# Kernel optimization log

Hardware: AMD Instinct MI355X
Metric: run time of the kernel (lower is better)

Reference implementation:

```python
import jax, jax.numpy as jnp
import numpy as np
from functools import partial

EPS = 1e-5
SCALE = 2
NUM_BLOCKS = 2


def _layernorm(x, g, b):
    mu = jnp.mean(x, axis=-1, keepdims=True)
    var = jnp.var(x, axis=-1, keepdims=True)
    return (x - mu) * jax.lax.rsqrt(var + EPS) * g + b


def _rwkv(tokens, td, Wk, Wv, Wr, Wo, ln_g, ln_b):
    # tokens: (B, N, C)
    x = _layernorm(tokens, ln_g, ln_b)
    k = jnp.einsum('bnc,oc->bno', x, Wk)
    v = jnp.einsum('bnc,oc->bno', x, Wv)
    r = jax.nn.sigmoid(jnp.einsum('bnc,oc->bno', x, Wr))
    decay = jnp.exp(-jax.nn.relu(td))  # (C,)

    def step(state, inp):
        kt, vt, rt = inp  # each (B, C)
        state = state * decay + kt
        return state, rt * (state + vt)

    B, N, C = tokens.shape
    init = jnp.zeros((B, C), dtype=tokens.dtype)
    # scan over token axis
    _, yT = jax.lax.scan(step, init, (k.transpose(1, 0, 2), v.transpose(1, 0, 2), r.transpose(1, 0, 2)))
    y = yT.transpose(1, 0, 2)  # (B, N, C)
    return jnp.einsum('bnc,oc->bno', y, Wo)


def reference(x, global_state, cond_gw, cond_gb, cond_bw, cond_bb,
              td, Wk, Wv, Wr, Wo, ln_g, ln_b, gp_w, gp_b, bp_w, bp_b):
    B, C, H, W = x.shape
    Hp, Wp = H * SCALE, W * SCALE
    # bilinear upsample, half-pixel centers == torch align_corners=False
    x_up = jax.image.resize(x, (B, C, Hp, Wp), method='bilinear')
    tokens = x_up.reshape(B, C, Hp * Wp).transpose(0, 2, 1)  # (B, N, C)
    # semantic conditioning (FiLM from global state)
    gamma = (global_state @ cond_gw.T + cond_gb)[:, None, :]
    beta = (global_state @ cond_bw.T + cond_bb)[:, None, :]
    tokens = tokens * (1.0 + gamma) + beta

    out = x_up
    cur = tokens
    for i in range(NUM_BLOCKS):
        if i > 0:
            cur = out.reshape(B, C, Hp * Wp).transpose(0, 2, 1)
        t = _rwkv(cur, td[i], Wk[i], Wv[i], Wr[i], Wo[i], ln_g[i], ln_b[i])
        g = jnp.einsum('bnc,oc->bno', t, gp_w[i]) + gp_b[i]
        bt = jnp.einsum('bnc,oc->bno', t, bp_w[i]) + bp_b[i]
        g = g.transpose(0, 2, 1).reshape(B, C, Hp, Wp)
        bt = bt.transpose(0, 2, 1).reshape(B, C, Hp, Wp)
        out = out * (1.0 + jnp.tanh(g)) + bt
    return out


def setup_inputs() -> dict:
    key = jax.random.key(0)
    ks = jax.random.split(key, 16)
    B, C, H, W = 8, 128, 64, 64
    w_scale = 0.02
    inp = {
        'x': jax.random.normal(ks[0], (B, C, H, W), jnp.float32),
        'global_state': jax.random.normal(ks[1], (B, C), jnp.float32),
        'cond_gw': jax.random.normal(ks[2], (C, C), jnp.float32) * w_scale,
        'cond_gb': jnp.zeros((C,), jnp.float32),
        'cond_bw': jax.random.normal(ks[3], (C, C), jnp.float32) * w_scale,
        'cond_bb': jnp.zeros((C,), jnp.float32),
        'td': jax.random.uniform(ks[4], (NUM_BLOCKS, C), jnp.float32),
        'Wk': jax.random.normal(ks[5], (NUM_BLOCKS, C, C), jnp.float32) * w_scale,
        'Wv': jax.random.normal(ks[6], (NUM_BLOCKS, C, C), jnp.float32) * w_scale,
        'Wr': jax.random.normal(ks[7], (NUM_BLOCKS, C, C), jnp.float32) * w_scale,
        'Wo': jax.random.normal(ks[8], (NUM_BLOCKS, C, C), jnp.float32) * w_scale,
        'ln_g': jnp.ones((NUM_BLOCKS, C), jnp.float32),
        'ln_b': jnp.zeros((NUM_BLOCKS, C), jnp.float32),
        'gp_w': jax.random.normal(ks[9], (NUM_BLOCKS, C, C), jnp.float32) * w_scale,
        'gp_b': jnp.zeros((NUM_BLOCKS, C), jnp.float32),
        'bp_w': jax.random.normal(ks[10], (NUM_BLOCKS, C, C), jnp.float32) * w_scale,
        'bp_b': jnp.zeros((NUM_BLOCKS, C), jnp.float32),
    }
    return inp
```

## Files before the change

kernel.cpp:

```cpp
#include <hip/hip_runtime.h>
#include <hip/hip_bf16.h>

#define BB 8
#define CC 128
#define NN 16384
#define MM (BB * NN)
#define NCH 128
#define CLN 128

typedef __attribute__((ext_vector_type(8))) short short8;
typedef __attribute__((ext_vector_type(4))) float floatx4;
typedef unsigned short u16;
typedef unsigned int u32;

__device__ __forceinline__ float bf2f(u16 h) {
  u32 u = ((u32)h) << 16;
  return __builtin_bit_cast(float, u);
}
__device__ __forceinline__ u16 f2bf(float f) {
  u32 u = __builtin_bit_cast(u32, f);
  u32 r = u + 0x7FFFu + ((u >> 16) & 1u);
  return (u16)(r >> 16);
}

__global__ void film_kernel(const float* __restrict__ gs, const float* __restrict__ gw,
                            const float* __restrict__ gb, const float* __restrict__ bw,
                            const float* __restrict__ bb, float* __restrict__ gamma,
                            float* __restrict__ beta) {
  int idx = blockIdx.x * 256 + threadIdx.x;
  int b = idx >> 7, c = idx & 127;
  float sg = 0.f, sb = 0.f;
  for (int j = 0; j < 128; ++j) {
    float g = gs[b * 128 + j];
    sg += g * gw[c * 128 + j];
    sb += g * bw[c * 128 + j];
  }
  gamma[idx] = sg + gb[c];
  beta[idx] = sb + bb[c];
}

__global__ void convert_kernel(const float* __restrict__ Wk, const float* __restrict__ Wv,
                               const float* __restrict__ Wr, const float* __restrict__ Wo,
                               const float* __restrict__ gp, const float* __restrict__ bp,
                               u16* __restrict__ dst) {
  int idx = blockIdx.x * 256 + threadIdx.x;
  int which = idx >> 15;
  int off = idx & 32767;
  const float* s;
  switch (which) {
    case 0: s = Wk; break; case 1: s = Wv; break; case 2: s = Wr; break;
    case 3: s = Wo; break; case 4: s = gp; break; default: s = bp; break;
  }
  dst[idx] = f2bf(s[off]);
}

template <int UPS>
__global__ __launch_bounds__(256) void prep_kernel(
    const float* __restrict__ src, const float* __restrict__ gamma,
    const float* __restrict__ beta, const float* __restrict__ lng,
    const float* __restrict__ lnb, float* __restrict__ outp, u16* __restrict__ xn) {
  __shared__ float tile[64][129];
  __shared__ float smu[64], srs[64];
  int bidx = blockIdx.x;
  int half = bidx & 1;
  int ho = (bidx >> 1) & 127;
  int b = bidx >> 8;
  int wo0 = half * 64;
  int tid = threadIdx.x;
  int tk = tid & 63;
  int wo = wo0 + tk;
  int c0 = tid >> 6;
  int j0 = 0, j1 = 0, i0 = 0, i1 = 0;
  float wy0 = 0.f, wy1 = 0.f, wx0 = 0.f, wx1 = 0.f;
  if (UPS) {
    int jj = ho >> 1;
    if ((ho & 1) == 0) { j0 = jj > 0 ? jj - 1 : 0; j1 = jj; wy0 = 0.25f; wy1 = 0.75f; }
    else               { j0 = jj; j1 = jj < 63 ? jj + 1 : 63; wy0 = 0.75f; wy1 = 0.25f; }
    int ii = wo >> 1;
    if ((wo & 1) == 0) { i0 = ii > 0 ? ii - 1 : 0; i1 = ii; wx0 = 0.25f; wx1 = 0.75f; }
    else               { i0 = ii; i1 = ii < 63 ? ii + 1 : 63; wx0 = 0.75f; wx1 = 0.25f; }
  }
  for (int it = 0; it < 32; ++it) {
    int c = it * 4 + c0;
    float v;
    if (UPS) {
      const float* xp = src + ((size_t)(b * 128 + c)) * 4096;
      v = wy0 * (wx0 * xp[j0 * 64 + i0] + wx1 * xp[j0 * 64 + i1]) +
          wy1 * (wx0 * xp[j1 * 64 + i0] + wx1 * xp[j1 * 64 + i1]);
      outp[((size_t)(b * 128 + c)) * 16384 + ho * 128 + wo] = v;
      v = v * (1.f + gamma[b * 128 + c]) + beta[b * 128 + c];
    } else {
      v = src[((size_t)(b * 128 + c)) * 16384 + ho * 128 + wo];
    }
    tile[tk][c] = v;
  }
  __syncthreads();
  {
    int token = tid >> 2, q = tid & 3;
    float s = 0.f, s2 = 0.f;
    for (int j = 0; j < 32; ++j) { float v = tile[token][q * 32 + j]; s += v; s2 += v * v; }
    s += __shfl_xor(s, 1); s2 += __shfl_xor(s2, 1);
    s += __shfl_xor(s, 2); s2 += __shfl_xor(s2, 2);
    if (q == 0) {
      float mu = s * 0.0078125f;
      float var = s2 * 0.0078125f - mu * mu;
      smu[token] = mu;
      srs[token] = rsqrtf(var + 1e-5f);
    }
  }
  __syncthreads();
  size_t base = ((size_t)b * 16384 + ho * 128 + wo0) * 128;
  for (int it = 0; it < 32; ++it) {
    int idx = it * 256 + tid;
    int token = idx >> 7, c = idx & 127;
    float v = (tile[token][c] - smu[token]) * srs[token] * lng[c] + lnb[c];
    xn[base + idx] = f2bf(v);
  }
}

__global__ __launch_bounds__(256) void gemm_S_kernel(
    const u16* __restrict__ A, const u16* __restrict__ W0,
    const float* __restrict__ td, float* __restrict__ Sbuf) {
  __shared__ u16 Alds[128 * 128];
  __shared__ float Sred[512];
  int tid = threadIdx.x;
  int wave = tid >> 6, lane = tid & 63;
  int l15 = lane & 15, l4 = lane >> 4;
  size_t row0 = (size_t)blockIdx.x * 128;
#pragma unroll
  for (int it = 0; it < 8; ++it) {
    int idx = it * 256 + tid;
    int rr = idx >> 4, s = idx & 15;
    uint4 d = *(const uint4*)(A + (row0 + rr) * 128 + s * 8);
    *(uint4*)(&Alds[rr * 128 + ((s ^ (rr & 15)) << 3)]) = d;
  }
  __syncthreads();
  floatx4 acc[2][8];
#pragma unroll
  for (int mi = 0; mi < 2; ++mi)
#pragma unroll
    for (int ni = 0; ni < 8; ++ni) acc[mi][ni] = (floatx4){0.f, 0.f, 0.f, 0.f};
#pragma unroll
  for (int kk = 0; kk < 4; ++kk) {
    int seg = kk * 4 + l4;
    short8 a0 = *(const short8*)(&Alds[(wave * 32 + l15) * 128 + ((seg ^ l15) << 3)]);
    short8 a1 = *(const short8*)(&Alds[(wave * 32 + 16 + l15) * 128 + ((seg ^ l15) << 3)]);
#pragma unroll
    for (int ni = 0; ni < 8; ++ni) {
      short8 bfr = *(const short8*)(W0 + (ni * 16 + l15) * 128 + kk * 32 + l4 * 8);
      acc[0][ni] = __builtin_amdgcn_mfma_f32_16x16x32_bf16(a0, bfr, acc[0][ni], 0, 0, 0);
      acc[1][ni] = __builtin_amdgcn_mfma_f32_16x16x32_bf16(a1, bfr, acc[1][ni], 0, 0, 0);
    }
  }
  int T0 = wave * 32 + l4 * 4;
#pragma unroll
  for (int ni = 0; ni < 8; ++ni) {
    int c = ni * 16 + l15;
    float a = fmaxf(td[c], 0.f);
    float E = __expf(-a * (float)(127 - T0));
    float r1 = __expf(a);
    float r16 = __expf(a * 16.f);
    float w = E, sum;
    sum  = w * acc[0][ni][0]; w *= r1;
    sum += w * acc[0][ni][1]; w *= r1;
    sum += w * acc[0][ni][2]; w *= r1;
    sum += w * acc[0][ni][3];
    w = E * r16;
    sum += w * acc[1][ni][0]; w *= r1;
    sum += w * acc[1][ni][1]; w *= r1;
    sum += w * acc[1][ni][2]; w *= r1;
    sum += w * acc[1][ni][3];
    sum += __shfl_xor(sum, 16);
    sum += __shfl_xor(sum, 32);
    if (l4 == 0) Sred[wave * 128 + c] = sum;
  }
  __syncthreads();
  if (tid < 128) {
    float s = Sred[tid] + Sred[128 + tid] + Sred[256 + tid] + Sred[384 + tid];
    Sbuf[(blockIdx.x & 127) * 1024 + (blockIdx.x >> 7) * 128 + tid] = s;
  }
}

__global__ __launch_bounds__(256) void scan2_kernel(const float* __restrict__ S,
                                                    const float* __restrict__ td,
                                                    float* __restrict__ init) {
  int wave = threadIdx.x >> 6, lane = threadIdx.x & 63;
  int bc = blockIdx.x * 4 + wave;
  int c = bc & 127;
  float a1 = __expf(-fmaxf(td[c], 0.f) * 128.f);
  float s0 = S[(2 * lane) * 1024 + bc];
  float s1 = S[(2 * lane + 1) * 1024 + bc];
  float s = s1 + a1 * s0;
  float a = a1 * a1;
  for (int off = 1; off < 64; off <<= 1) {
    float ss = __shfl_up(s, off);
    float aa = __shfl_up(a, off);
    if (lane >= off) { s = s + a * ss; a = a * aa; }
  }
  float e = __shfl_up(s, 1);
  if (lane == 0) e = 0.f;
  init[(2 * lane) * 1024 + bc] = e;
  init[(2 * lane + 1) * 1024 + bc] = a1 * e + s0;
}

__global__ __launch_bounds__(256) void gemm_y_kernel(
    const u16* __restrict__ A, const u16* __restrict__ Wv_, const u16* __restrict__ Wr_,
    const u16* __restrict__ Wk_, const float* __restrict__ td,
    const float* __restrict__ init_, u16* __restrict__ outY) {
  __shared__ u16 Alds[128 * 128];
  __shared__ u16 Wlds[128 * 128];
  __shared__ float SWT[512];
  __shared__ float ILS[128];
  int tid = threadIdx.x;
  int wave = tid >> 6, lane = tid & 63;
  int l15 = lane & 15, l4 = lane >> 4;
  size_t row0 = (size_t)blockIdx.x * 128;
  int bI = blockIdx.x >> 7, chunkI = blockIdx.x & 127;
  if (tid < 128) ILS[tid] = init_[chunkI * 1024 + bI * 128 + tid];

#pragma unroll
  for (int it = 0; it < 8; ++it) {
    int idx = it * 256 + tid;
    int rr = idx >> 4, s = idx & 15;
    uint4 d = *(const uint4*)(A + (row0 + rr) * 128 + s * 8);
    *(uint4*)(&Alds[rr * 128 + ((s ^ (rr & 15)) << 3)]) = d;
  }
#pragma unroll
  for (int it = 0; it < 8; ++it) {
    int idx = it * 256 + tid;
    int rr = idx >> 4, s = idx & 15;
    uint4 d = *(const uint4*)(Wv_ + rr * 128 + s * 8);
    *(uint4*)(&Wlds[rr * 128 + ((s ^ (rr & 15)) << 3)]) = d;
  }
  float dd[8], d4a[8];
#pragma unroll
  for (int ni = 0; ni < 8; ++ni) {
    float a = fmaxf(td[ni * 16 + l15], 0.f);
    float d = __expf(-a);
    dd[ni] = d;
    float d2 = d * d;
    d4a[ni] = d2 * d2;
  }
  __syncthreads();

  floatx4 accv[2][8];
#pragma unroll
  for (int mi = 0; mi < 2; ++mi)
#pragma unroll
    for (int ni = 0; ni < 8; ++ni) accv[mi][ni] = (floatx4){0.f, 0.f, 0.f, 0.f};
#pragma unroll
  for (int kk = 0; kk < 4; ++kk) {
    int seg = kk * 4 + l4;
    short8 a0 = *(const short8*)(&Alds[(wave * 32 + l15) * 128 + ((seg ^ l15) << 3)]);
    short8 a1 = *(const short8*)(&Alds[(wave * 32 + 16 + l15) * 128 + ((seg ^ l15) << 3)]);
#pragma unroll
    for (int ni = 0; ni < 8; ++ni) {
      short8 bfr = *(const short8*)(&Wlds[(ni * 16 + l15) * 128 + ((seg ^ l15) << 3)]);
      accv[0][ni] = __builtin_amdgcn_mfma_f32_16x16x32_bf16(a0, bfr, accv[0][ni], 0, 0, 0);
      accv[1][ni] = __builtin_amdgcn_mfma_f32_16x16x32_bf16(a1, bfr, accv[1][ni], 0, 0, 0);
    }
  }
  __syncthreads();
#pragma unroll
  for (int it = 0; it < 8; ++it) {
    int idx = it * 256 + tid;
    int rr = idx >> 4, s = idx & 15;
    uint4 d = *(const uint4*)(Wr_ + rr * 128 + s * 8);
    *(uint4*)(&Wlds[rr * 128 + ((s ^ (rr & 15)) << 3)]) = d;
  }
  __syncthreads();
  floatx4 accr[2][8];
#pragma unroll
  for (int mi = 0; mi < 2; ++mi)
#pragma unroll
    for (int ni = 0; ni < 8; ++ni) accr[mi][ni] = (floatx4){0.f, 0.f, 0.f, 0.f};
#pragma unroll
  for (int kk = 0; kk < 4; ++kk) {
    int seg = kk * 4 + l4;
    short8 a0 = *(const short8*)(&Alds[(wave * 32 + l15) * 128 + ((seg ^ l15) << 3)]);
    short8 a1 = *(const short8*)(&Alds[(wave * 32 + 16 + l15) * 128 + ((seg ^ l15) << 3)]);
#pragma unroll
    for (int ni = 0; ni < 8; ++ni) {
      short8 bfr = *(const short8*)(&Wlds[(ni * 16 + l15) * 128 + ((seg ^ l15) << 3)]);
      accr[0][ni] = __builtin_amdgcn_mfma_f32_16x16x32_bf16(a0, bfr, accr[0][ni], 0, 0, 0);
      accr[1][ni] = __builtin_amdgcn_mfma_f32_16x16x32_bf16(a1, bfr, accr[1][ni], 0, 0, 0);
    }
  }
  u32 rvp[2][8][2], rp[2][8][2];
#pragma unroll
  for (int mi = 0; mi < 2; ++mi) {
#pragma unroll
    for (int ni = 0; ni < 8; ++ni) {
      float rs[4], rv[4];
#pragma unroll
      for (int j = 0; j < 4; ++j) {
        float sg = 1.f / (1.f + __expf(-accr[mi][ni][j]));
        rs[j] = sg;
        rv[j] = sg * accv[mi][ni][j];
      }
      rvp[mi][ni][0] = (u32)f2bf(rv[0]) | ((u32)f2bf(rv[1]) << 16);
      rvp[mi][ni][1] = (u32)f2bf(rv[2]) | ((u32)f2bf(rv[3]) << 16);
      rp[mi][ni][0] = (u32)f2bf(rs[0]) | ((u32)f2bf(rs[1]) << 16);
      rp[mi][ni][1] = (u32)f2bf(rs[2]) | ((u32)f2bf(rs[3]) << 16);
    }
  }
  __syncthreads();
#pragma unroll
  for (int it = 0; it < 8; ++it) {
    int idx = it * 256 + tid;
    int rr = idx >> 4, s = idx & 15;
    uint4 d = *(const uint4*)(Wk_ + rr * 128 + s * 8);
    *(uint4*)(&Wlds[rr * 128 + ((s ^ (rr & 15)) << 3)]) = d;
  }
  __syncthreads();
  floatx4 acck[2][8];
#pragma unroll
  for (int mi = 0; mi < 2; ++mi)
#pragma unroll
    for (int ni = 0; ni < 8; ++ni) acck[mi][ni] = (floatx4){0.f, 0.f, 0.f, 0.f};
#pragma unroll
  for (int kk = 0; kk < 4; ++kk) {
    int seg = kk * 4 + l4;
    short8 a0 = *(const short8*)(&Alds[(wave * 32 + l15) * 128 + ((seg ^ l15) << 3)]);
    short8 a1 = *(const short8*)(&Alds[(wave * 32 + 16 + l15) * 128 + ((seg ^ l15) << 3)]);
#pragma unroll
    for (int ni = 0; ni < 8; ++ni) {
      short8 bfr = *(const short8*)(&Wlds[(ni * 16 + l15) * 128 + ((seg ^ l15) << 3)]);
      acck[0][ni] = __builtin_amdgcn_mfma_f32_16x16x32_bf16(a0, bfr, acck[0][ni], 0, 0, 0);
      acck[1][ni] = __builtin_amdgcn_mfma_f32_16x16x32_bf16(a1, bfr, acck[1][ni], 0, 0, 0);
    }
  }
  float Elr[2][8];
  float B0r[8];
#pragma unroll
  for (int ni = 0; ni < 8; ++ni) {
    float d = dd[ni], d4 = d4a[ni];
    float d8 = d4 * d4, d16 = d8 * d8;
    float I[2];
#pragma unroll
    for (int mi = 0; mi < 2; ++mi) {
      float p0 = acck[mi][ni][0];
      float p1 = d * p0 + acck[mi][ni][1];
      float p2 = d * p1 + acck[mi][ni][2];
      float p3 = d * p2 + acck[mi][ni][3];
      acck[mi][ni][0] = p0; acck[mi][ni][1] = p1;
      acck[mi][ni][2] = p2; acck[mi][ni][3] = p3;
      float Iv = p3;
      float t1 = __shfl_up(Iv, 16);
      if (l4 >= 1) Iv += d4 * t1;
      float t2 = __shfl_up(Iv, 32);
      if (l4 >= 2) Iv += d8 * t2;
      float ex = __shfl_up(Iv, 16);
      Elr[mi][ni] = (l4 == 0) ? 0.f : ex;
      I[mi] = Iv;
    }
    float B0 = __shfl(I[0], 48 + l15);
    float B1 = __shfl(I[1], 48 + l15);
    B0r[ni] = B0;
    if (l4 == 0) SWT[wave * 128 + ni * 16 + l15] = B1 + d16 * B0;
  }
  __syncthreads();
  u16* YW = Wlds;
#pragma unroll
  for (int ni = 0; ni < 8; ++ni) {
    int c = ni * 16 + l15;
    float d = dd[ni], d4 = d4a[ni];
    float d8 = d4 * d4, d12 = d8 * d4, d16 = d8 * d8, d32 = d16 * d16;
    float e = ILS[c];
#pragma unroll
    for (int wv = 0; wv < 3; ++wv)
      if (wv < wave) e = e * d32 + SWT[wv * 128 + c];
    float d4l = (l4 == 0) ? 1.f : ((l4 == 1) ? d4 : ((l4 == 2) ? d8 : d12));
#pragma unroll
    for (int mi = 0; mi < 2; ++mi) {
      float Emi = (mi == 0) ? e : (e * d16 + B0r[ni]);
      float Sb = Elr[mi][ni] + d4l * Emi;
      float w = d;
#pragma unroll
      for (int j = 0; j < 4; ++j) {
        float s = acck[mi][ni][j] + w * Sb;
        w *= d;
        float rvv = bf2f((u16)(rvp[mi][ni][j >> 1] >> ((j & 1) * 16)));
        float rss = bf2f((u16)(rp[mi][ni][j >> 1] >> ((j & 1) * 16)));
        float y = rvv + rss * s;
        int row = wave * 32 + mi * 16 + l4 * 4 + j;
        int colsw = c ^ (((row >> 2) & 3) << 4);
        YW[row * 128 + colsw] = f2bf(y);
      }
    }
  }
  __syncthreads();
#pragma unroll
  for (int it = 0; it < 8; ++it) {
    int idx = it * 256 + tid;
    int row = idx >> 4, cb = (idx & 15) * 8;
    int csw = cb ^ (((row >> 2) & 3) << 4);
    uint4 dv = *(const uint4*)(&YW[row * 128 + csw]);
    *(uint4*)(outY + (row0 + row) * 128 + cb) = dv;
  }
}

__global__ __launch_bounds__(512, 4) void tail_kernel(
    const u16* __restrict__ yl,
    const u16* __restrict__ Wo, const u16* __restrict__ Wg, const u16* __restrict__ Wb,
    const float* __restrict__ gpb, const float* __restrict__ bpb,
    float* __restrict__ outp) {
  __shared__ u32 SMEM[8192];
  u16* Y = (u16*)SMEM;
  u16* T2 = (u16*)SMEM;
  u32* MB = SMEM;

  int tid = threadIdx.x;
  int wave = tid >> 6, lane = tid & 63;
  int l15 = lane & 15, l4 = lane >> 4;
  int b = blockIdx.x >> 7;
  int chunk = blockIdx.x & 127;
  size_t ebase = ((size_t)b * 16384 + (size_t)chunk * 128) * 128;

#pragma unroll
  for (int it = 0; it < 4; ++it) {
    int idx = it * 512 + tid;
    int t = idx >> 4;
    int c8 = (idx & 15) * 8;
    uint4 yv = *(const uint4*)(yl + ebase + (size_t)t * 128 + c8);
    *(uint4*)(&Y[t * 128 + (((c8 >> 3) ^ (t & 15)) << 3)]) = yv;
  }
  __syncthreads();

  int ob = wave * 16;
  short8 wof[4];
#pragma unroll
  for (int kk = 0; kk < 4; ++kk)
    wof[kk] = *(const short8*)(Wo + (ob + l15) * 128 + kk * 32 + l4 * 8);
  floatx4 acc[8];
#pragma unroll
  for (int ni = 0; ni < 8; ++ni) acc[ni] = (floatx4){0.f, 0.f, 0.f, 0.f};
#pragma unroll
  for (int kk = 0; kk < 4; ++kk) {
    int seg = kk * 4 + l4;
#pragma unroll
    for (int ni = 0; ni < 8; ++ni) {
      short8 yf = *(const short8*)(&Y[(ni * 16 + l15) * 128 + ((seg ^ l15) << 3)]);
      acc[ni] = __builtin_amdgcn_mfma_f32_16x16x32_bf16(wof[kk], yf, acc[ni], 0, 0, 0);
    }
  }
  __syncthreads();

#pragma unroll
  for (int ni = 0; ni < 8; ++ni) {
    int tok = ni * 16 + l15;
#pragma unroll
    for (int j = 0; j < 4; j += 2) {
      int o = ob + l4 * 4 + j;
      u32 pack = (u32)f2bf(acc[ni][j]) | ((u32)f2bf(acc[ni][j + 1]) << 16);
      int pos = tok * 128 + ((((o >> 3) ^ (tok & 15)) << 3) | (o & 7));
      *(u32*)(T2 + pos) = pack;
    }
  }
  __syncthreads();

  short8 wgf[4], wbf2[4];
#pragma unroll
  for (int kk = 0; kk < 4; ++kk) {
    wgf[kk]  = *(const short8*)(Wg + (ob + l15) * 128 + kk * 32 + l4 * 8);
    wbf2[kk] = *(const short8*)(Wb + (ob + l15) * 128 + kk * 32 + l4 * 8);
  }
  floatx4 ag[8], ab[8];
#pragma unroll
  for (int ni = 0; ni < 8; ++ni) {
    ag[ni] = (floatx4){0.f, 0.f, 0.f, 0.f};
    ab[ni] = (floatx4){0.f, 0.f, 0.f, 0.f};
  }
#pragma unroll
  for (int kk = 0; kk < 4; ++kk) {
    int seg = kk * 4 + l4;
#pragma unroll
    for (int ni = 0; ni < 8; ++ni) {
      short8 tf = *(const short8*)(&T2[(ni * 16 + l15) * 128 + ((seg ^ l15) << 3)]);
      ag[ni] = __builtin_amdgcn_mfma_f32_16x16x32_bf16(wgf[kk], tf, ag[ni], 0, 0, 0);
      ab[ni] = __builtin_amdgcn_mfma_f32_16x16x32_bf16(wbf2[kk], tf, ab[ni], 0, 0, 0);
    }
  }
  __syncthreads();

#pragma unroll
  for (int h = 0; h < 2; ++h) {
    if ((wave >> 2) == h) {
      int orel0 = (wave & 3) * 16;
#pragma unroll
      for (int ni = 0; ni < 8; ++ni) {
        int tok = ni * 16 + l15;
#pragma unroll
        for (int j = 0; j < 4; ++j) {
          int orel = orel0 + l4 * 4 + j;
          int o = h * 64 + orel;
          float g = ag[ni][j] + gpb[o];
          float t1 = __expf(2.f * g);
          float m = 2.f - 2.f / (t1 + 1.f);
          float bt = ab[ni][j] + bpb[o];
          int rot = ((orel & 3) << 2) | ((orel >> 2) & 3);
          MB[orel * 128 + ((((tok >> 3) ^ rot) << 3) | (tok & 7))] =
              (u32)f2bf(m) | ((u32)f2bf(bt) << 16);
        }
      }
    }
    __syncthreads();
#pragma unroll
    for (int it = 0; it < 2; ++it) {
      int idx = it * 512 + tid;
      int orel = idx >> 4, seg = idx & 15;
      int o = h * 64 + orel;
      int rot = ((orel & 3) << 2) | ((orel >> 2) & 3);
      int sp = ((seg ^ rot) << 3);
      uint4 mb0 = *(const uint4*)(&MB[orel * 128 + sp]);
      uint4 mb1 = *(const uint4*)(&MB[orel * 128 + sp + 4]);
      float* op = outp + ((size_t)(b * 128 + o)) * 16384 + chunk * 128 + seg * 8;
      float4 o0 = *(float4*)op;
      float4 o1 = *(float4*)(op + 4);
      o0.x = o0.x * bf2f((u16)(mb0.x & 0xffff)) + bf2f((u16)(mb0.x >> 16));
      o0.y = o0.y * bf2f((u16)(mb0.y & 0xffff)) + bf2f((u16)(mb0.y >> 16));
      o0.z = o0.z * bf2f((u16)(mb0.z & 0xffff)) + bf2f((u16)(mb0.z >> 16));
      o0.w = o0.w * bf2f((u16)(mb0.w & 0xffff)) + bf2f((u16)(mb0.w >> 16));
      o1.x = o1.x * bf2f((u16)(mb1.x & 0xffff)) + bf2f((u16)(mb1.x >> 16));
      o1.y = o1.y * bf2f((u16)(mb1.y & 0xffff)) + bf2f((u16)(mb1.y >> 16));
      o1.z = o1.z * bf2f((u16)(mb1.z & 0xffff)) + bf2f((u16)(mb1.z >> 16));
      o1.w = o1.w * bf2f((u16)(mb1.w & 0xffff)) + bf2f((u16)(mb1.w >> 16));
      *(float4*)op = o0;
      *(float4*)(op + 4) = o1;
    }
    __syncthreads();
  }
}

extern "C" void kernel_launch(void* const* d_in, const int* in_sizes, int n_in,
                              void* d_out, int out_size, void* d_ws, size_t ws_size,
                              hipStream_t stream) {
  const float* x        = (const float*)d_in[0];
  const float* gs       = (const float*)d_in[1];
  const float* cond_gw  = (const float*)d_in[2];
  const float* cond_gb  = (const float*)d_in[3];
  const float* cond_bw  = (const float*)d_in[4];
  const float* cond_bb  = (const float*)d_in[5];
  const float* td       = (const float*)d_in[6];
  const float* Wk       = (const float*)d_in[7];
  const float* Wv       = (const float*)d_in[8];
  const float* Wr       = (const float*)d_in[9];
  const float* Wo       = (const float*)d_in[10];
  const float* ln_g     = (const float*)d_in[11];
  const float* ln_b     = (const float*)d_in[12];
  const float* gp_w     = (const float*)d_in[13];
  const float* gp_b     = (const float*)d_in[14];
  const float* bp_w     = (const float*)d_in[15];
  const float* bp_b     = (const float*)d_in[16];
  float* outp = (float*)d_out;

  char* w = (char*)d_ws;
  float* gamma = (float*)w; w += 4096;
  float* beta  = (float*)w; w += 4096;
  u16* wbf     = (u16*)w;   w += 6 * 2 * 16384 * sizeof(u16);
  u16* xn      = (u16*)w;   w += (size_t)MM * 128 * sizeof(u16);
  u16* ybuf    = (u16*)w;   w += (size_t)MM * 128 * sizeof(u16);
  float* Sbuf  = (float*)w; w += NCH * 1024 * sizeof(float);
  float* ibuf  = (float*)w; w += NCH * 1024 * sizeof(float);

  film_kernel<<<4, 256, 0, stream>>>(gs, cond_gw, cond_gb, cond_bw, cond_bb, gamma, beta);
  convert_kernel<<<768, 256, 0, stream>>>(Wk, Wv, Wr, Wo, gp_w, bp_w, wbf);

  for (int blk = 0; blk < 2; ++blk) {
    const u16* bWk = wbf + 0 * 32768 + blk * 16384;
    const u16* bWv = wbf + 1 * 32768 + blk * 16384;
    const u16* bWr = wbf + 2 * 32768 + blk * 16384;
    const u16* bWo = wbf + 3 * 32768 + blk * 16384;
    const u16* bGp = wbf + 4 * 32768 + blk * 16384;
    const u16* bBp = wbf + 5 * 32768 + blk * 16384;
    const float* tdi = td + blk * 128;

    if (blk == 0)
      prep_kernel<1><<<2048, 256, 0, stream>>>(x, gamma, beta, ln_g, ln_b, outp, xn);
    else
      prep_kernel<0><<<2048, 256, 0, stream>>>(outp, nullptr, nullptr, ln_g + 128,
                                               ln_b + 128, nullptr, xn);

    gemm_S_kernel<<<1024, 256, 0, stream>>>(xn, bWk, tdi, Sbuf);
    scan2_kernel<<<256, 256, 0, stream>>>(Sbuf, tdi, ibuf);
    gemm_y_kernel<<<1024, 256, 0, stream>>>(xn, bWv, bWr, bWk, tdi, ibuf, ybuf);
    tail_kernel<<<1024, 512, 0, stream>>>(ybuf, bWo, bGp, bBp,
                                          gp_b + blk * 128, bp_b + blk * 128, outp);
  }
}
```

Measured before the change: 320.5 us.

## Halve scan chunk length and retile gemm_y to 64-row blocks with per-wave channels

The chunked linear-recurrence scan now uses 64-token chunks instead of 128. gemm_S emits two half-chunk sums per block and stages Wk in LDS. scan2 combines four chunk sums per lane, and gemm_y runs 2048 blocks of 64 rows, each wave owning 32 output channels. This removes the cross-wave SWT reduction, the LDS weight staging in gemm_y and its extra syncs, and lowers LDS use to raise occupancy. In exchange, each wave reads weights directly from global/L2, and intermediate s and r values are packed to bf16 before the final combine.

```diff
diff --git a/kernel.cpp b/kernel.cpp
--- a/kernel.cpp
+++ b/kernel.cpp
@@ -5,8 +5,8 @@
 #define CC 128
 #define NN 16384
 #define MM (BB * NN)
-#define NCH 128
-#define CLN 128
+#define NCH 256
+#define CLN 64
 
 typedef __attribute__((ext_vector_type(8))) short short8;
 typedef __attribute__((ext_vector_type(4))) float floatx4;
@@ -122,6 +122,7 @@
     const u16* __restrict__ A, const u16* __restrict__ W0,
     const float* __restrict__ td, float* __restrict__ Sbuf) {
   __shared__ u16 Alds[128 * 128];
+  __shared__ u16 Wlds[128 * 128];
   __shared__ float Sred[512];
   int tid = threadIdx.x;
   int wave = tid >> 6, lane = tid & 63;
@@ -134,6 +135,13 @@
     uint4 d = *(const uint4*)(A + (row0 + rr) * 128 + s * 8);
     *(uint4*)(&Alds[rr * 128 + ((s ^ (rr & 15)) << 3)]) = d;
   }
+#pragma unroll
+  for (int it = 0; it < 8; ++it) {
+    int idx = it * 256 + tid;
+    int rr = idx >> 4, s = idx & 15;
+    uint4 d = *(const uint4*)(W0 + rr * 128 + s * 8);
+    *(uint4*)(&Wlds[rr * 128 + ((s ^ (rr & 15)) << 3)]) = d;
+  }
   __syncthreads();
   floatx4 acc[2][8];
 #pragma unroll
@@ -147,17 +155,17 @@
     short8 a1 = *(const short8*)(&Alds[(wave * 32 + 16 + l15) * 128 + ((seg ^ l15) << 3)]);
 #pragma unroll
     for (int ni = 0; ni < 8; ++ni) {
-      short8 bfr = *(const short8*)(W0 + (ni * 16 + l15) * 128 + kk * 32 + l4 * 8);
+      short8 bfr = *(const short8*)(&Wlds[(ni * 16 + l15) * 128 + ((seg ^ l15) << 3)]);
       acc[0][ni] = __builtin_amdgcn_mfma_f32_16x16x32_bf16(a0, bfr, acc[0][ni], 0, 0, 0);
       acc[1][ni] = __builtin_amdgcn_mfma_f32_16x16x32_bf16(a1, bfr, acc[1][ni], 0, 0, 0);
     }
   }
-  int T0 = wave * 32 + l4 * 4;
+  int T0h = (wave & 1) * 32 + l4 * 4;
 #pragma unroll
   for (int ni = 0; ni < 8; ++ni) {
     int c = ni * 16 + l15;
     float a = fmaxf(td[c], 0.f);
-    float E = __expf(-a * (float)(127 - T0));
+    float E = __expf(-a * (float)(63 - T0h));
     float r1 = __expf(a);
     float r16 = __expf(a * 16.f);
     float w = E, sum;
@@ -176,8 +184,10 @@
   }
   __syncthreads();
   if (tid < 128) {
-    float s = Sred[tid] + Sred[128 + tid] + Sred[256 + tid] + Sred[384 + tid];
-    Sbuf[(blockIdx.x & 127) * 1024 + (blockIdx.x >> 7) * 128 + tid] = s;
+    int hc0 = (blockIdx.x & 127) * 2;
+    int bo = (blockIdx.x >> 7) * 128 + tid;
+    Sbuf[(size_t)hc0 * 1024 + bo]       = Sred[tid] + Sred[128 + tid];
+    Sbuf[(size_t)(hc0 + 1) * 1024 + bo] = Sred[256 + tid] + Sred[384 + tid];
   }
 }
 
@@ -187,11 +197,14 @@
   int wave = threadIdx.x >> 6, lane = threadIdx.x & 63;
   int bc = blockIdx.x * 4 + wave;
   int c = bc & 127;
-  float a1 = __expf(-fmaxf(td[c], 0.f) * 128.f);
-  float s0 = S[(2 * lane) * 1024 + bc];
-  float s1 = S[(2 * lane + 1) * 1024 + bc];
-  float s = s1 + a1 * s0;
-  float a = a1 * a1;
+  float a1 = __expf(-fmaxf(td[c], 0.f) * 64.f);
+  float s0 = S[(size_t)(4 * lane + 0) * 1024 + bc];
+  float s1 = S[(size_t)(4 * lane + 1) * 1024 + bc];
+  float s2 = S[(size_t)(4 * lane + 2) * 1024 + bc];
+  float s3 = S[(size_t)(4 * lane + 3) * 1024 + bc];
+  float a2 = a1 * a1;
+  float T = s3 + a1 * s2 + a2 * (s1 + a1 * s0);
+  float s = T, a = a2 * a2;
   for (int off = 1; off < 64; off <<= 1) {
     float ss = __shfl_up(s, off);
     float aa = __shfl_up(a, off);
@@ -199,199 +212,172 @@
   }
   float e = __shfl_up(s, 1);
   if (lane == 0) e = 0.f;
-  init[(2 * lane) * 1024 + bc] = e;
-  init[(2 * lane + 1) * 1024 + bc] = a1 * e + s0;
-}
-
-__global__ __launch_bounds__(256) void gemm_y_kernel(
-    const u16* __restrict__ A, const u16* __restrict__ Wv_, const u16* __restrict__ Wr_,
-    const u16* __restrict__ Wk_, const float* __restrict__ td,
-    const float* __restrict__ init_, u16* __restrict__ outY) {
-  __shared__ u16 Alds[128 * 128];
-  __shared__ u16 Wlds[128 * 128];
-  __shared__ float SWT[512];
+  init[(size_t)(4 * lane + 0) * 1024 + bc] = e;
+  float e1 = a1 * e + s0;  init[(size_t)(4 * lane + 1) * 1024 + bc] = e1;
+  float e2 = a1 * e1 + s1; init[(size_t)(4 * lane + 2) * 1024 + bc] = e2;
+  float e3 = a1 * e2 + s2; init[(size_t)(4 * lane + 3) * 1024 + bc] = e3;
+}
+
+__global__ __launch_bounds__(256, 4) void gemm_y_kernel(
+    const u16* __restrict__ xn, const u16* __restrict__ Wv_,
+    const u16* __restrict__ Wr_, const u16* __restrict__ Wk_,
+    const float* __restrict__ td, const float* __restrict__ init_,
+    u16* __restrict__ outY) {
+  __shared__ u16 Alds[64 * 128];
   __shared__ float ILS[128];
   int tid = threadIdx.x;
   int wave = tid >> 6, lane = tid & 63;
   int l15 = lane & 15, l4 = lane >> 4;
-  size_t row0 = (size_t)blockIdx.x * 128;
-  int bI = blockIdx.x >> 7, chunkI = blockIdx.x & 127;
-  if (tid < 128) ILS[tid] = init_[chunkI * 1024 + bI * 128 + tid];
-
-#pragma unroll
-  for (int it = 0; it < 8; ++it) {
+  size_t row0 = (size_t)blockIdx.x * 64;
+  int bI = blockIdx.x >> 8, hcI = blockIdx.x & 255;
+  if (tid < 128) ILS[tid] = init_[(size_t)hcI * 1024 + bI * 128 + tid];
+#pragma unroll
+  for (int it = 0; it < 4; ++it) {
     int idx = it * 256 + tid;
     int rr = idx >> 4, s = idx & 15;
-    uint4 d = *(const uint4*)(A + (row0 + rr) * 128 + s * 8);
+    uint4 d = *(const uint4*)(xn + (row0 + rr) * 128 + s * 8);
     *(uint4*)(&Alds[rr * 128 + ((s ^ (rr & 15)) << 3)]) = d;
   }
-#pragma unroll
-  for (int it = 0; it < 8; ++it) {
-    int idx = it * 256 + tid;
-    int rr = idx >> 4, s = idx & 15;
-    uint4 d = *(const uint4*)(Wv_ + rr * 128 + s * 8);
-    *(uint4*)(&Wlds[rr * 128 + ((s ^ (rr & 15)) << 3)]) = d;
-  }
-  float dd[8], d4a[8];
-#pragma unroll
-  for (int ni = 0; ni < 8; ++ni) {
-    float a = fmaxf(td[ni * 16 + l15], 0.f);
+  int ob = wave * 32;
+  float dd[2], d4a[2];
+#pragma unroll
+  for (int ni = 0; ni < 2; ++ni) {
+    float a = fmaxf(td[ob + ni * 16 + l15], 0.f);
     float d = __expf(-a);
     dd[ni] = d;
-    float d2 = d * d;
-    d4a[ni] = d2 * d2;
-  }
-  __syncthreads();
-
-  floatx4 accv[2][8];
-#pragma unroll
-  for (int mi = 0; mi < 2; ++mi)
-#pragma unroll
-    for (int ni = 0; ni < 8; ++ni) accv[mi][ni] = (floatx4){0.f, 0.f, 0.f, 0.f};
+    d4a[ni] = d * d * d * d;
+  }
+  __syncthreads();
+
+  floatx4 acc[4][2];
+#pragma unroll
+  for (int mi = 0; mi < 4; ++mi)
+#pragma unroll
+    for (int ni = 0; ni < 2; ++ni) acc[mi][ni] = (floatx4){0.f, 0.f, 0.f, 0.f};
 #pragma unroll
   for (int kk = 0; kk < 4; ++kk) {
-    int seg = kk * 4 + l4;
-    short8 a0 = *(const short8*)(&Alds[(wave * 32 + l15) * 128 + ((seg ^ l15) << 3)]);
-    short8 a1 = *(const short8*)(&Alds[(wave * 32 + 16 + l15) * 128 + ((seg ^ l15) << 3)]);
-#pragma unroll
-    for (int ni = 0; ni < 8; ++ni) {
-      short8 bfr = *(const short8*)(&Wlds[(ni * 16 + l15) * 128 + ((seg ^ l15) << 3)]);
-      accv[0][ni] = __builtin_amdgcn_mfma_f32_16x16x32_bf16(a0, bfr, accv[0][ni], 0, 0, 0);
-      accv[1][ni] = __builtin_amdgcn_mfma_f32_16x16x32_bf16(a1, bfr, accv[1][ni], 0, 0, 0);
-    }
-  }
-  __syncthreads();
-#pragma unroll
-  for (int it = 0; it < 8; ++it) {
-    int idx = it * 256 + tid;
-    int rr = idx >> 4, s = idx & 15;
-    uint4 d = *(const uint4*)(Wr_ + rr * 128 + s * 8);
-    *(uint4*)(&Wlds[rr * 128 + ((s ^ (rr & 15)) << 3)]) = d;
-  }
-  __syncthreads();
-  floatx4 accr[2][8];
-#pragma unroll
-  for (int mi = 0; mi < 2; ++mi)
-#pragma unroll
-    for (int ni = 0; ni < 8; ++ni) accr[mi][ni] = (floatx4){0.f, 0.f, 0.f, 0.f};
+    short8 w0 = *(const short8*)(Wk_ + (ob + l15) * 128 + kk * 32 + l4 * 8);
+    short8 w1 = *(const short8*)(Wk_ + (ob + 16 + l15) * 128 + kk * 32 + l4 * 8);
+#pragma unroll
+    for (int mi = 0; mi < 4; ++mi) {
+      short8 af = *(const short8*)(&Alds[(mi * 16 + l15) * 128 + (((kk * 4 + l4) ^ l15) << 3)]);
+      acc[mi][0] = __builtin_amdgcn_mfma_f32_16x16x32_bf16(af, w0, acc[mi][0], 0, 0, 0);
+      acc[mi][1] = __builtin_amdgcn_mfma_f32_16x16x32_bf16(af, w1, acc[mi][1], 0, 0, 0);
+    }
+  }
+
+  u32 sp[4][2][2];
+  {
+    float Elr[4][2], Bm[4][2];
+#pragma unroll
+    for (int ni = 0; ni < 2; ++ni) {
+      float d = dd[ni], d4 = d4a[ni];
+      float d8 = d4 * d4;
+#pragma unroll
+      for (int mi = 0; mi < 4; ++mi) {
+        float p0 = acc[mi][ni][0];
+        float p1 = d * p0 + acc[mi][ni][1];
+        float p2 = d * p1 + acc[mi][ni][2];
+        float p3 = d * p2 + acc[mi][ni][3];
+        acc[mi][ni][0] = p0; acc[mi][ni][1] = p1;
+        acc[mi][ni][2] = p2; acc[mi][ni][3] = p3;
+        float Iv = p3;
+        float t1 = __shfl_up(Iv, 16);
+        if (l4 >= 1) Iv += d4 * t1;
+        float t2 = __shfl_up(Iv, 32);
+        if (l4 >= 2) Iv += d8 * t2;
+        float ex = __shfl_up(Iv, 16);
+        Elr[mi][ni] = (l4 == 0) ? 0.f : ex;
+        Bm[mi][ni] = __shfl(Iv, 48 + l15);
+      }
+    }
+#pragma unroll
+    for (int ni = 0; ni < 2; ++ni) {
+      float d = dd[ni], d4 = d4a[ni];
+      float d8 = d4 * d4, d12 = d8 * d4, d16 = d8 * d8;
+      float d4l = (l4 == 0) ? 1.f : ((l4 == 1) ? d4 : ((l4 == 2) ? d8 : d12));
+      float e = ILS[ob + ni * 16 + l15];
+#pragma unroll
+      for (int mi = 0; mi < 4; ++mi) {
+        float Sb = Elr[mi][ni] + d4l * e;
+        float w = d;
+        float s0 = acc[mi][ni][0] + w * Sb; w *= d;
+        float s1 = acc[mi][ni][1] + w * Sb; w *= d;
+        float s2 = acc[mi][ni][2] + w * Sb; w *= d;
+        float s3 = acc[mi][ni][3] + w * Sb;
+        sp[mi][ni][0] = (u32)f2bf(s0) | ((u32)f2bf(s1) << 16);
+        sp[mi][ni][1] = (u32)f2bf(s2) | ((u32)f2bf(s3) << 16);
+        e = e * d16 + Bm[mi][ni];
+      }
+    }
+  }
+
+  u32 rp[4][2][2];
+  {
+#pragma unroll
+    for (int mi = 0; mi < 4; ++mi)
+#pragma unroll
+      for (int ni = 0; ni < 2; ++ni) acc[mi][ni] = (floatx4){0.f, 0.f, 0.f, 0.f};
+#pragma unroll
+    for (int kk = 0; kk < 4; ++kk) {
+      short8 w0 = *(const short8*)(Wr_ + (ob + l15) * 128 + kk * 32 + l4 * 8);
+      short8 w1 = *(const short8*)(Wr_ + (ob + 16 + l15) * 128 + kk * 32 + l4 * 8);
+#pragma unroll
+      for (int mi = 0; mi < 4; ++mi) {
+        short8 af = *(const short8*)(&Alds[(mi * 16 + l15) * 128 + (((kk * 4 + l4) ^ l15) << 3)]);
+        acc[mi][0] = __builtin_amdgcn_mfma_f32_16x16x32_bf16(af, w0, acc[mi][0], 0, 0, 0);
+        acc[mi][1] = __builtin_amdgcn_mfma_f32_16x16x32_bf16(af, w1, acc[mi][1], 0, 0, 0);
+      }
+    }
+#pragma unroll
+    for (int mi = 0; mi < 4; ++mi)
+#pragma unroll
+      for (int ni = 0; ni < 2; ++ni) {
+        float r0 = 1.f / (1.f + __expf(-acc[mi][ni][0]));
+        float r1 = 1.f / (1.f + __expf(-acc[mi][ni][1]));
+        float r2 = 1.f / (1.f + __expf(-acc[mi][ni][2]));
+        float r3 = 1.f / (1.f + __expf(-acc[mi][ni][3]));
+        rp[mi][ni][0] = (u32)f2bf(r0) | ((u32)f2bf(r1) << 16);
+        rp[mi][ni][1] = (u32)f2bf(r2) | ((u32)f2bf(r3) << 16);
+      }
+  }
+
+#pragma unroll
+  for (int mi = 0; mi < 4; ++mi)
+#pragma unroll
+    for (int ni = 0; ni < 2; ++ni) acc[mi][ni] = (floatx4){0.f, 0.f, 0.f, 0.f};
 #pragma unroll
   for (int kk = 0; kk < 4; ++kk) {
-    int seg = kk * 4 + l4;
-    short8 a0 = *(const short8*)(&Alds[(wave * 32 + l15) * 128 + ((seg ^ l15) << 3)]);
-    short8 a1 = *(const short8*)(&Alds[(wave * 32 + 16 + l15) * 128 + ((seg ^ l15) << 3)]);
-#pragma unroll
-    for (int ni = 0; ni < 8; ++ni) {
-      short8 bfr = *(const short8*)(&Wlds[(ni * 16 + l15) * 128 + ((seg ^ l15) << 3)]);
-      accr[0][ni] = __builtin_amdgcn_mfma_f32_16x16x32_bf16(a0, bfr, accr[0][ni], 0, 0, 0);
-      accr[1][ni] = __builtin_amdgcn_mfma_f32_16x16x32_bf16(a1, bfr, accr[1][ni], 0, 0, 0);
-    }
-  }
-  u32 rvp[2][8][2], rp[2][8][2];
-#pragma unroll
-  for (int mi = 0; mi < 2; ++mi) {
-#pragma unroll
-    for (int ni = 0; ni < 8; ++ni) {
-      float rs[4], rv[4];
+    short8 w0 = *(const short8*)(Wv_ + (ob + l15) * 128 + kk * 32 + l4 * 8);
+    short8 w1 = *(const short8*)(Wv_ + (ob + 16 + l15) * 128 + kk * 32 + l4 * 8);
+#pragma unroll
+    for (int mi = 0; mi < 4; ++mi) {
+      short8 af = *(const short8*)(&Alds[(mi * 16 + l15) * 128 + (((kk * 4 + l4) ^ l15) << 3)]);
+      acc[mi][0] = __builtin_amdgcn_mfma_f32_16x16x32_bf16(af, w0, acc[mi][0], 0, 0, 0);
+      acc[mi][1] = __builtin_amdgcn_mfma_f32_16x16x32_bf16(af, w1, acc[mi][1], 0, 0, 0);
+    }
+  }
+  __syncthreads();
+
+  u16* YW = Alds;
+#pragma unroll
+  for (int mi = 0; mi < 4; ++mi)
+#pragma unroll
+    for (int ni = 0; ni < 2; ++ni) {
+      int c = ob + ni * 16 + l15;
 #pragma unroll
       for (int j = 0; j < 4; ++j) {
-        float sg = 1.f / (1.f + __expf(-accr[mi][ni][j]));
-        rs[j] = sg;
-        rv[j] = sg * accv[mi][ni][j];
-      }
-      rvp[mi][ni][0] = (u32)f2bf(rv[0]) | ((u32)f2bf(rv[1]) << 16);
-      rvp[mi][ni][1] = (u32)f2bf(rv[2]) | ((u32)f2bf(rv[3]) << 16);
-      rp[mi][ni][0] = (u32)f2bf(rs[0]) | ((u32)f2bf(rs[1]) << 16);
-      rp[mi][ni][1] = (u32)f2bf(rs[2]) | ((u32)f2bf(rs[3]) << 16);
-    }
-  }
-  __syncthreads();
-#pragma unroll
-  for (int it = 0; it < 8; ++it) {
-    int idx = it * 256 + tid;
-    int rr = idx >> 4, s = idx & 15;
-    uint4 d = *(const uint4*)(Wk_ + rr * 128 + s * 8);
-    *(uint4*)(&Wlds[rr * 128 + ((s ^ (rr & 15)) << 3)]) = d;
-  }
-  __syncthreads();
-  floatx4 acck[2][8];
-#pragma unroll
-  for (int mi = 0; mi < 2; ++mi)
-#pragma unroll
-    for (int ni = 0; ni < 8; ++ni) acck[mi][ni] = (floatx4){0.f, 0.f, 0.f, 0.f};
-#pragma unroll
-  for (int kk = 0; kk < 4; ++kk) {
-    int seg = kk * 4 + l4;
-    short8 a0 = *(const short8*)(&Alds[(wave * 32 + l15) * 128 + ((seg ^ l15) << 3)]);
-    short8 a1 = *(const short8*)(&Alds[(wave * 32 + 16 + l15) * 128 + ((seg ^ l15) << 3)]);
-#pragma unroll
-    for (int ni = 0; ni < 8; ++ni) {
-      short8 bfr = *(const short8*)(&Wlds[(ni * 16 + l15) * 128 + ((seg ^ l15) << 3)]);
-      acck[0][ni] = __builtin_amdgcn_mfma_f32_16x16x32_bf16(a0, bfr, acck[0][ni], 0, 0, 0);
-      acck[1][ni] = __builtin_amdgcn_mfma_f32_16x16x32_bf16(a1, bfr, acck[1][ni], 0, 0, 0);
-    }
-  }
-  float Elr[2][8];
-  float B0r[8];
-#pragma unroll
-  for (int ni = 0; ni < 8; ++ni) {
-    float d = dd[ni], d4 = d4a[ni];
-    float d8 = d4 * d4, d16 = d8 * d8;
-    float I[2];
-#pragma unroll
-    for (int mi = 0; mi < 2; ++mi) {
-      float p0 = acck[mi][ni][0];
-      float p1 = d * p0 + acck[mi][ni][1];
-      float p2 = d * p1 + acck[mi][ni][2];
-      float p3 = d * p2 + acck[mi][ni][3];
-      acck[mi][ni][0] = p0; acck[mi][ni][1] = p1;
-      acck[mi][ni][2] = p2; acck[mi][ni][3] = p3;
-      float Iv = p3;
-      float t1 = __shfl_up(Iv, 16);
-      if (l4 >= 1) Iv += d4 * t1;
-      float t2 = __shfl_up(Iv, 32);
-      if (l4 >= 2) Iv += d8 * t2;
-      float ex = __shfl_up(Iv, 16);
-      Elr[mi][ni] = (l4 == 0) ? 0.f : ex;
-      I[mi] = Iv;
-    }
-    float B0 = __shfl(I[0], 48 + l15);
-    float B1 = __shfl(I[1], 48 + l15);
-    B0r[ni] = B0;
-    if (l4 == 0) SWT[wave * 128 + ni * 16 + l15] = B1 + d16 * B0;
-  }
-  __syncthreads();
-  u16* YW = Wlds;
-#pragma unroll
-  for (int ni = 0; ni < 8; ++ni) {
-    int c = ni * 16 + l15;
-    float d = dd[ni], d4 = d4a[ni];
-    float d8 = d4 * d4, d12 = d8 * d4, d16 = d8 * d8, d32 = d16 * d16;
-    float e = ILS[c];
-#pragma unroll
-    for (int wv = 0; wv < 3; ++wv)
-      if (wv < wave) e = e * d32 + SWT[wv * 128 + c];
-    float d4l = (l4 == 0) ? 1.f : ((l4 == 1) ? d4 : ((l4 == 2) ? d8 : d12));
-#pragma unroll
-    for (int mi = 0; mi < 2; ++mi) {
-      float Emi = (mi == 0) ? e : (e * d16 + B0r[ni]);
-      float Sb = Elr[mi][ni] + d4l * Emi;
-      float w = d;
-#pragma unroll
-      for (int j = 0; j < 4; ++j) {
-        float s = acck[mi][ni][j] + w * Sb;
-        w *= d;
-        float rvv = bf2f((u16)(rvp[mi][ni][j >> 1] >> ((j & 1) * 16)));
-        float rss = bf2f((u16)(rp[mi][ni][j >> 1] >> ((j & 1) * 16)));
-        float y = rvv + rss * s;
-        int row = wave * 32 + mi * 16 + l4 * 4 + j;
+        float s = bf2f((u16)(sp[mi][ni][j >> 1] >> ((j & 1) * 16)));
+        float rs = bf2f((u16)(rp[mi][ni][j >> 1] >> ((j & 1) * 16)));
+        float y = rs * (s + acc[mi][ni][j]);
+        int row = mi * 16 + l4 * 4 + j;
         int colsw = c ^ (((row >> 2) & 3) << 4);
         YW[row * 128 + colsw] = f2bf(y);
       }
     }
-  }
-  __syncthreads();
-#pragma unroll
-  for (int it = 0; it < 8; ++it) {
+  __syncthreads();
+#pragma unroll
+  for (int it = 0; it < 4; ++it) {
     int idx = it * 256 + tid;
     int row = idx >> 4, cb = (idx & 15) * 8;
     int csw = cb ^ (((row >> 2) & 3) << 4);
@@ -560,8 +546,8 @@
   u16* wbf     = (u16*)w;   w += 6 * 2 * 16384 * sizeof(u16);
   u16* xn      = (u16*)w;   w += (size_t)MM * 128 * sizeof(u16);
   u16* ybuf    = (u16*)w;   w += (size_t)MM * 128 * sizeof(u16);
-  float* Sbuf  = (float*)w; w += NCH * 1024 * sizeof(float);
-  float* ibuf  = (float*)w; w += NCH * 1024 * sizeof(float);
+  float* Sbuf  = (float*)w; w += (size_t)NCH * 1024 * sizeof(float);
+  float* ibuf  = (float*)w; w += (size_t)NCH * 1024 * sizeof(float);
 
   film_kernel<<<4, 256, 0, stream>>>(gs, cond_gw, cond_gb, cond_bw, cond_bb, gamma, beta);
   convert_kernel<<<768, 256, 0, stream>>>(Wk, Wv, Wr, Wo, gp_w, bp_w, wbf);
@@ -583,7 +569,7 @@
 
     gemm_S_kernel<<<1024, 256, 0, stream>>>(xn, bWk, tdi, Sbuf);
     scan2_kernel<<<256, 256, 0, stream>>>(Sbuf, tdi, ibuf);
-    gemm_y_kernel<<<1024, 256, 0, stream>>>(xn, bWv, bWr, bWk, tdi, ibuf, ybuf);
+    gemm_y_kernel<<<2048, 256, 0, stream>>>(xn, bWv, bWr, bWk, tdi, ibuf, ybuf);
     tail_kernel<<<1024, 512, 0, stream>>>(ybuf, bWo, bGp, bBp,
                                           gp_b + blk * 128, bp_b + blk * 128, outp);
   }
```

New measurement: 309.6 us. 3.4% less time.
